# Performance work log

Measured on AMD Instinct MI355X. Metric: run time of the kernel, lower is better.

Reference implementation:

```python
import jax, jax.numpy as jnp
import numpy as np

NP_, NS_ = 100000, 10000      # num pdrugs / seffect nodes
FPD, FSE = 512, 768           # raw feature dims
H = 64                        # hidden_channels
E = 1_600_000                 # message-passing edges
L = 1_000_000                 # labeled edges (pos+neg)


def setup_inputs() -> dict:
    key = jax.random.key(0)
    ks = jax.random.split(key, 40)
    f32 = jnp.float32

    def nrm(k, shape, scale=0.05):
        return jax.random.normal(k, shape, f32) * scale

    inp = {}
    inp['x_pdrugs'] = jax.random.normal(ks[0], (NP_, FPD), f32)
    inp['x_seffect'] = jax.random.normal(ks[1], (NS_, FSE), f32)
    inp['node_id_pd'] = jnp.arange(NP_)
    inp['node_id_se'] = jnp.arange(NS_)
    inp['edge_index'] = jnp.stack([
        jax.random.randint(ks[2], (E,), 0, NP_),
        jax.random.randint(ks[3], (E,), 0, NS_)])
    # positive labeled edges + negative-sampled edges (label 0)
    inp['edge_label_index'] = jnp.stack([
        jax.random.randint(ks[4], (L,), 0, NP_),
        jax.random.randint(ks[5], (L,), 0, NS_)])
    inp['edge_label'] = jnp.concatenate(
        [jnp.ones(L // 2, f32), jnp.zeros(L - L // 2, f32)])

    # input projections + node embeddings
    inp['W_pd'] = nrm(ks[6], (FPD, H)); inp['b_pd'] = jnp.zeros((H,), f32)
    inp['W_se'] = nrm(ks[7], (FSE, H)); inp['b_se'] = jnp.zeros((H,), f32)
    inp['emb_pd'] = nrm(ks[8], (NP_, H), 1.0)
    inp['emb_se'] = nrm(ks[9], (NS_, H), 1.0)

    # hetero SAGEConv params: 2 layers x 2 edge types (p2s, s2p)
    i = 10
    for lyr in (1, 2):
        for et in ('p2s', 's2p'):
            inp[f'c{lyr}_{et}_Wl'] = nrm(ks[i], (H, H)); i += 1
            inp[f'c{lyr}_{et}_bl'] = jnp.zeros((H,), f32)
            inp[f'c{lyr}_{et}_Wr'] = nrm(ks[i], (H, H)); i += 1
    return inp


def _sage(x_src, x_dst, src_idx, dst_idx, n_dst, Wl, bl, Wr):
    # SAGEConv: lin_l(mean_j x_src[j]) + lin_r(x_dst)
    msg = x_src[src_idx]                                   # [E, H] gather
    agg = jax.ops.segment_sum(msg, dst_idx, num_segments=n_dst)
    deg = jax.ops.segment_sum(jnp.ones((src_idx.shape[0],), x_src.dtype),
                              dst_idx, num_segments=n_dst)
    mean = agg / jnp.clip(deg, 1.0)[:, None]
    return mean @ Wl + bl + x_dst @ Wr


def reference(x_pdrugs, x_seffect, edge_label,
              W_pd, b_pd, W_se, b_se, emb_pd, emb_se,
              c1_p2s_Wl, c1_p2s_bl, c1_p2s_Wr,
              c1_s2p_Wl, c1_s2p_bl, c1_s2p_Wr,
              c2_p2s_Wl, c2_p2s_bl, c2_p2s_Wr,
              c2_s2p_Wl, c2_s2p_bl, c2_s2p_Wr,
              node_id_pd, node_id_se, edge_index, edge_label_index):
    src, dst = edge_index[0], edge_index[1]  # pdrugs -> seffect

    # embed + linear fusion
    h_pd = x_pdrugs @ W_pd + b_pd + emb_pd[node_id_pd]
    h_se = x_seffect @ W_se + b_se + emb_se[node_id_se]

    # hetero GNN layer 1 (relu)
    se1 = jax.nn.relu(_sage(h_pd, h_se, src, dst, NS_, c1_p2s_Wl, c1_p2s_bl, c1_p2s_Wr))
    pd1 = jax.nn.relu(_sage(h_se, h_pd, dst, src, NP_, c1_s2p_Wl, c1_s2p_bl, c1_s2p_Wr))

    # hetero GNN layer 2 (no activation)
    se2 = _sage(pd1, se1, src, dst, NS_, c2_p2s_Wl, c2_p2s_bl, c2_p2s_Wr)
    pd2 = _sage(se1, pd1, dst, src, NP_, c2_s2p_Wl, c2_s2p_bl, c2_s2p_Wr)

    # edge-wise gather-dot classifier
    pred = jnp.sum(pd2[edge_label_index[0]] * se2[edge_label_index[1]], axis=-1)
    return (pred, edge_label)
```

## Files before the change

### kernel.cpp

```cpp
#include <hip/hip_runtime.h>

namespace {

constexpr int NP = 100000;
constexpr int NS = 10000;
constexpr int EC = 1600000;
constexpr int LC = 1000000;

constexpr int SH_S = 6;
constexpr int SH_P = 9;
constexpr int NBS = (NS + 63) >> SH_S;
constexpr int NBP = (NP + 511) >> SH_P;
constexpr int CHUNK = 8192;
constexpr int NBLK = (EC + CHUNK - 1) / CHUNK;
constexpr int LBLK = (LC + CHUNK - 1) / CHUNK;

typedef short i16x8 __attribute__((ext_vector_type(8)));
typedef float f32x4 __attribute__((ext_vector_type(4)));

__device__ inline ushort f2bf(float f) {
  unsigned u = __float_as_uint(f);
  u += 0x7FFFu + ((u >> 16) & 1u);
  return (ushort)(u >> 16);
}
__device__ inline float bflo(uint v) { return __uint_as_float(v << 16); }
__device__ inline float bfhi(uint v) { return __uint_as_float(v & 0xffff0000u); }

__device__ inline i16x8 pack8(float4 a, float4 b) {
  i16x8 r;
  r[0] = (short)f2bf(a.x);
  r[1] = (short)f2bf(a.y);
  r[2] = (short)f2bf(a.z);
  r[3] = (short)f2bf(a.w);
  r[4] = (short)f2bf(b.x);
  r[5] = (short)f2bf(b.y);
  r[6] = (short)f2bf(b.z);
  r[7] = (short)f2bf(b.w);
  return r;
}


__global__ void __launch_bounds__(256) k_bcount(const int* __restrict__ src,
                                                const int* __restrict__ dst,
                                                const int* __restrict__ li0,
                                                int* __restrict__ bcntS,
                                                int* __restrict__ bcntP,
                                                int* __restrict__ bcntL, int E, int L) {
  __shared__ int hS[256];
  __shared__ int hP[256];
  const int t = threadIdx.x;
  if ((int)blockIdx.x >= NBLK) {
    hS[t] = 0;
    __syncthreads();
    const int base = ((int)blockIdx.x - NBLK) * CHUNK;
    const int end = min(base + CHUNK, L);
    for (int e = base + t; e < end; e += 256) atomicAdd(&hS[li0[e] >> SH_P], 1);
    __syncthreads();
    if (t < NBP && hS[t]) atomicAdd(&bcntL[t], hS[t]);
    return;
  }
  hS[t] = 0;
  hP[t] = 0;
  __syncthreads();
  const int base = blockIdx.x * CHUNK;
  const int end = min(base + CHUNK, E);
  for (int e = base + t; e < end; e += 256) {
    atomicAdd(&hS[dst[e] >> SH_S], 1);
    atomicAdd(&hP[src[e] >> SH_P], 1);
  }
  __syncthreads();
  if (t < NBS && hS[t]) atomicAdd(&bcntS[t], hS[t]);
  if (t < NBP && hP[t]) atomicAdd(&bcntP[t], hP[t]);
}

__global__ void __launch_bounds__(256) k_bscan(const int* __restrict__ bcntS,
                                               const int* __restrict__ bcntP,
                                               const int* __restrict__ bcntL,
                                               int* __restrict__ gbaseS,
                                               int* __restrict__ gbaseP,
                                               int* __restrict__ gcurS,
                                               int* __restrict__ gcurP,
                                               int* __restrict__ gcurL) {
  __shared__ int s[256];
  const int t = threadIdx.x;
  int v = (t < NBS) ? bcntS[t] : 0;
  s[t] = v;
  __syncthreads();
  for (int off = 1; off < 256; off <<= 1) {
    int u = (t >= off) ? s[t - off] : 0;
    __syncthreads();
    s[t] += u;
    __syncthreads();
  }
  if (t < NBS) {
    int ex = s[t] - v;
    gbaseS[t] = ex;
    gcurS[t] = ex;
  }
  __syncthreads();
  v = (t < NBP) ? bcntP[t] : 0;
  s[t] = v;
  __syncthreads();
  for (int off = 1; off < 256; off <<= 1) {
    int u = (t >= off) ? s[t - off] : 0;
    __syncthreads();
    s[t] += u;
    __syncthreads();
  }
  if (t < NBP) {
    int ex = s[t] - v;
    gbaseP[t] = ex;
    gcurP[t] = ex;
  }
  __syncthreads();
  v = (t < NBP) ? bcntL[t] : 0;
  s[t] = v;
  __syncthreads();
  for (int off = 1; off < 256; off <<= 1) {
    int u = (t >= off) ? s[t - off] : 0;
    __syncthreads();
    s[t] += u;
    __syncthreads();
  }
  if (t < NBP) gcurL[t] = s[t] - v;
}

__global__ void __launch_bounds__(256) k_bscatter(const int* __restrict__ src,
                                                  const int* __restrict__ dst,
                                                  const int* __restrict__ li0,
                                                  int* __restrict__ gcurS,
                                                  int* __restrict__ gcurP,
                                                  int* __restrict__ gcurL,
                                                  int* __restrict__ tmpS,
                                                  int* __restrict__ tmpP,
                                                  int2* __restrict__ tmpL, int E, int L) {
  __shared__ int hS[256];
  __shared__ int hP[256];
  const int t = threadIdx.x;
  if ((int)blockIdx.x >= NBLK) {
    hS[t] = 0;
    __syncthreads();
    const int base = ((int)blockIdx.x - NBLK) * CHUNK;
    const int end = min(base + CHUNK, L);
    for (int e = base + t; e < end; e += 256) atomicAdd(&hS[li0[e] >> SH_P], 1);
    __syncthreads();
    int myBase = 0;
    if (t < NBP) {
      int c = hS[t];
      myBase = c ? atomicAdd(&gcurL[t], c) : 0;
    }
    __syncthreads();
    if (t < NBP) hS[t] = myBase;
    __syncthreads();
    for (int e = base + t; e < end; e += 256) {
      const int a = li0[e];
      int p = atomicAdd(&hS[a >> SH_P], 1);
      tmpL[p] = make_int2(a, e);
    }
    return;
  }
  hS[t] = 0;
  hP[t] = 0;
  __syncthreads();
  const int base = blockIdx.x * CHUNK;
  const int end = min(base + CHUNK, E);
  for (int e = base + t; e < end; e += 256) {
    atomicAdd(&hS[dst[e] >> SH_S], 1);
    atomicAdd(&hP[src[e] >> SH_P], 1);
  }
  __syncthreads();
  int myBaseS = 0, myBaseP = 0;
  if (t < NBS) {
    int c = hS[t];
    myBaseS = c ? atomicAdd(&gcurS[t], c) : 0;
  }
  if (t < NBP) {
    int c = hP[t];
    myBaseP = c ? atomicAdd(&gcurP[t], c) : 0;
  }
  __syncthreads();
  if (t < NBS) hS[t] = myBaseS;
  if (t < NBP) hP[t] = myBaseP;
  __syncthreads();
  for (int e = base + t; e < end; e += 256) {
    const int d = dst[e];
    const int s = src[e];
    int p = atomicAdd(&hS[d >> SH_S], 1);
    tmpS[p] = ((d & 63) << 17) | s;
    int q = atomicAdd(&hP[s >> SH_P], 1);
    tmpP[q] = ((s & 511) << 14) | d;
  }
}

template <int NN, int LBITS>
__global__ void __launch_bounds__(256) k_bfinal(const int* __restrict__ tmp,
                                                const int* __restrict__ gbase,
                                                const int* __restrict__ bcnt,
                                                int shift, int Nnodes,
                                                int* __restrict__ rowptr,
                                                int* __restrict__ deg,
                                                int* __restrict__ col) {
  __shared__ int ldeg[NN];
  __shared__ int lscan[512];
  const int b = blockIdx.x;
  const int t = threadIdx.x;
  const int n0 = b << shift;
  const int base = gbase[b];
  const int cnt = bcnt[b];
  for (int i = t; i < NN; i += 256) ldeg[i] = 0;
  __syncthreads();
  for (int j = t; j < cnt; j += 256) atomicAdd(&ldeg[tmp[base + j] >> LBITS], 1);
  __syncthreads();
  for (int i = t; i < 512; i += 256) lscan[i] = (i < NN) ? ldeg[i] : 0;
  __syncthreads();
  for (int off = 1; off < 512; off <<= 1) {
    const int i0 = t, i1 = t + 256;
    const int v0 = (i0 >= off) ? lscan[i0 - off] : 0;
    const int v1 = (i1 >= off) ? lscan[i1 - off] : 0;
    __syncthreads();
    lscan[i0] += v0;
    lscan[i1] += v1;
    __syncthreads();
  }
  for (int i = t; i < NN; i += 256) {
    const int n = n0 + i;
    if (n < Nnodes) {
      const int dg = ldeg[i];
      rowptr[n] = base + lscan[i] - dg;
      deg[n] = dg;
    }
  }
  __syncthreads();
  for (int i = t; i < NN; i += 256) lscan[i] -= ldeg[i];
  __syncthreads();
  for (int j = t; j < cnt; j += 256) {
    const int v = tmp[base + j];
    const int p = atomicAdd(&lscan[v >> LBITS], 1);
    col[base + p] = v & ((1 << LBITS) - 1);
  }
}


struct WtJob {
  const float* src;
  ushort* dst;
  int K;
  int stride;
  int off;
};
struct WtJobs {
  WtJob j[10];
};

__global__ void __launch_bounds__(256) k_wt_all(WtJobs jobs) {
  int e = blockIdx.x * 256 + threadIdx.x;
#pragma unroll
  for (int i = 0; i < 10; i++) {
    const int K = jobs.j[i].K;
    const int sz = K * 64;
    if (e < sz) {
      const int n = e / K;
      const int k = e - n * K;
      jobs.j[i].dst[(size_t)n * jobs.j[i].stride + jobs.j[i].off + k] =
          f2bf(jobs.j[i].src[(size_t)k * 64 + n]);
      return;
    }
    e -= sz;
  }
}


struct GJob {
  const void* A0;
  const void* A1;
  int KA0, sA0, sA1, K;
  const ushort* Wt;
  const float* bias;
  const float* emb;
  const int* nid;
  void* out;
  int M;
  int nblk;
};

template <bool RELU, bool EMB, bool ABF16, bool OBF16>
__global__ void __launch_bounds__(256) k_fgemm(GJob ja, GJob jb) {
  const bool sec = (int)blockIdx.x >= ja.nblk;
  const GJob j = sec ? jb : ja;
  const int bid = sec ? ((int)blockIdx.x - ja.nblk) : (int)blockIdx.x;
  const int t = threadIdx.x;
  const int lane = t & 63;
  const int w = t >> 6;
  const int m16 = lane & 15;
  const int q = lane >> 4;
  const int M = j.M;
  const int K = j.K;
  const int KA0 = j.KA0;
  const int row0 = bid * 64 + w * 16;
  const int gr = min(row0 + m16, M - 1);

  f32x4 acc[4];
#pragma unroll
  for (int nt = 0; nt < 4; nt++) acc[nt] = {0.f, 0.f, 0.f, 0.f};

  const int ksteps = K >> 6;
#pragma unroll 2
  for (int ks = 0; ks < ksteps; ks++) {
    const int k0 = ks << 6;
    i16x8 a0, a1;
    if constexpr (ABF16) {
      const int ka = k0 + q * 8;
      const ushort* p0 = (ka < KA0)
                             ? ((const ushort*)j.A0 + (size_t)gr * j.sA0 + ka)
                             : ((const ushort*)j.A1 + (size_t)gr * j.sA1 + (ka - KA0));
      const int kb = ka + 32;
      const ushort* p1 = (kb < KA0)
                             ? ((const ushort*)j.A0 + (size_t)gr * j.sA0 + kb)
                             : ((const ushort*)j.A1 + (size_t)gr * j.sA1 + (kb - KA0));
      a0 = *reinterpret_cast<const i16x8*>(p0);
      a1 = *reinterpret_cast<const i16x8*>(p1);
    } else {
      const float* pa = (const float*)j.A0 + (size_t)gr * j.sA0 + k0 + q * 8;
      const float4 f0 = *reinterpret_cast<const float4*>(pa);
      const float4 f1 = *reinterpret_cast<const float4*>(pa + 4);
      const float4 g0 = *reinterpret_cast<const float4*>(pa + 32);
      const float4 g1 = *reinterpret_cast<const float4*>(pa + 36);
      a0 = pack8(f0, f1);
      a1 = pack8(g0, g1);
    }
#pragma unroll
    for (int nt = 0; nt < 4; nt++) {
      const ushort* wb = j.Wt + (size_t)(nt * 16 + m16) * K + k0 + q * 8;
      const i16x8 b0 = *reinterpret_cast<const i16x8*>(wb);
      const i16x8 b1 = *reinterpret_cast<const i16x8*>(wb + 32);
      acc[nt] = __builtin_amdgcn_mfma_f32_16x16x32_bf16(a0, b0, acc[nt], 0, 0, 0);
      acc[nt] = __builtin_amdgcn_mfma_f32_16x16x32_bf16(a1, b1, acc[nt], 0, 0, 0);
    }
  }

  int grow[4];
  int nrow[4];
#pragma unroll
  for (int r = 0; r < 4; r++) {
    grow[r] = bid * 64 + w * 16 + q * 4 + r;
    nrow[r] = (EMB && grow[r] < M) ? j.nid[grow[r]] : 0;
  }
#pragma unroll
  for (int nt = 0; nt < 4; nt++) {
    const int colv = nt * 16 + m16;
    const float bv = j.bias[colv];
#pragma unroll
    for (int r = 0; r < 4; r++) {
      if (grow[r] < M) {
        float v = acc[nt][r] + bv;
        if (EMB) v += j.emb[(size_t)nrow[r] * 64 + colv];
        if (RELU) v = fmaxf(v, 0.f);
        if (OBF16)
          ((ushort*)j.out)[(size_t)grow[r] * 64 + colv] = f2bf(v);
        else
          ((float*)j.out)[(size_t)grow[r] * 64 + colv] = v;
      }
    }
  }
}


__global__ void __launch_bounds__(256) k_agg2(
    const ushort* __restrict__ hS,
    const ushort* __restrict__ hP,
    const int* __restrict__ rpS, const int* __restrict__ degS, const int* __restrict__ colS,
    const int* __restrict__ rpP, const int* __restrict__ degP, const int* __restrict__ colP,
    ushort* __restrict__ outS,
    ushort* __restrict__ outP
) {
  int g = blockIdx.x * 4 + (threadIdx.x >> 6);
  const uint* hu;
  const int* rp;
  const int* deg;
  const int* col;
  uint* out;
  int node;
  if (g < NS) {
    hu = (const uint*)hS; rp = rpS; deg = degS; col = colS; out = (uint*)outS;
    node = g;
  } else {
    node = g - NS;
    if (node >= NP) return;
    hu = (const uint*)hP; rp = rpP; deg = degP; col = colP; out = (uint*)outP;
  }
  const int lane = threadIdx.x & 63;
  const int c = lane & 31;
  const int half = lane >> 5;
  const int beg = rp[node];
  const int cnt = deg[node];
  float a0 = 0.f, a1 = 0.f;
  int jj = 0;
  for (; jj + 16 <= cnt; jj += 16) {
    int n[8];
#pragma unroll
    for (int u = 0; u < 8; u++) n[u] = col[beg + jj + 2 * u + half];
#pragma unroll
    for (int u = 0; u < 8; u++) {
      const uint v = hu[(size_t)n[u] * 32 + c];
      a0 += bflo(v);
      a1 += bfhi(v);
    }
  }
  for (; jj + 2 <= cnt; jj += 2) {
    const uint v = hu[(size_t)col[beg + jj + half] * 32 + c];
    a0 += bflo(v);
    a1 += bfhi(v);
  }
  if (jj < cnt && half == 0) {
    const uint v = hu[(size_t)col[beg + jj] * 32 + c];
    a0 += bflo(v);
    a1 += bfhi(v);
  }
  a0 += __shfl_xor(a0, 32);
  a1 += __shfl_xor(a1, 32);
  if (half == 0) {
    const float d = (cnt > 0) ? (float)cnt : 1.f;
    const uint o = (uint)f2bf(a0 / d) | ((uint)f2bf(a1 / d) << 16);
    out[(size_t)node * 32 + c] = o;
  }
}


__global__ void __launch_bounds__(256) k_classify(const float* __restrict__ pd2,
                                                  const float* __restrict__ se2,
                                                  const int2* __restrict__ tmpL,
                                                  const int* __restrict__ i1,
                                                  const float* __restrict__ elabel,
                                                  float* __restrict__ outF, int L,
                                                  int nClsBlk) {
  if ((int)blockIdx.x >= nClsBlk) {
    const int i = ((int)blockIdx.x - nClsBlk) * 256 + threadIdx.x;
    if (i < L / 4)
      reinterpret_cast<float4*>(outF + L)[i] =
          reinterpret_cast<const float4*>(elabel)[i];
    return;
  }
  const int e = blockIdx.x * 16 + (threadIdx.x >> 4);
  if (e >= L) return;
  const int l16 = threadIdx.x & 15;
  const int2 pr = tmpL[e];
  const int a = pr.x;
  const int idx = pr.y;
  const int b = i1[idx];
  const float4 va = *reinterpret_cast<const float4*>(&pd2[(size_t)a * 64 + l16 * 4]);
  const float4 vb = *reinterpret_cast<const float4*>(&se2[(size_t)b * 64 + l16 * 4]);
  float v = va.x * vb.x + va.y * vb.y + va.z * vb.z + va.w * vb.w;
  v += __shfl_xor(v, 1, 16);
  v += __shfl_xor(v, 2, 16);
  v += __shfl_xor(v, 4, 16);
  v += __shfl_xor(v, 8, 16);
  if (l16 == 0) outF[idx] = v;
}

}

extern "C" void kernel_launch(void* const* d_in, const int* in_sizes, int n_in,
                              void* d_out, int out_size, void* d_ws, size_t ws_size,
                              hipStream_t stream) {
  (void)in_sizes; (void)n_in; (void)out_size; (void)ws_size;
  const float* x_pd = (const float*)d_in[0];
  const float* x_se = (const float*)d_in[1];
  const int* nid_pd = (const int*)d_in[2];
  const int* nid_se = (const int*)d_in[3];
  const int* eidx = (const int*)d_in[4];
  const int* elidx = (const int*)d_in[5];
  const float* elabel = (const float*)d_in[6];
  const float* W_pd = (const float*)d_in[7];
  const float* b_pd = (const float*)d_in[8];
  const float* W_se = (const float*)d_in[9];
  const float* b_se = (const float*)d_in[10];
  const float* emb_pd = (const float*)d_in[11];
  const float* emb_se = (const float*)d_in[12];
  const float* c1_p2s_Wl = (const float*)d_in[13];
  const float* c1_p2s_bl = (const float*)d_in[14];
  const float* c1_p2s_Wr = (const float*)d_in[15];
  const float* c1_s2p_Wl = (const float*)d_in[16];
  const float* c1_s2p_bl = (const float*)d_in[17];
  const float* c1_s2p_Wr = (const float*)d_in[18];
  const float* c2_p2s_Wl = (const float*)d_in[19];
  const float* c2_p2s_bl = (const float*)d_in[20];
  const float* c2_p2s_Wr = (const float*)d_in[21];
  const float* c2_s2p_Wl = (const float*)d_in[22];
  const float* c2_s2p_bl = (const float*)d_in[23];
  const float* c2_s2p_Wr = (const float*)d_in[24];

  const int* src = eidx;
  const int* dst = eidx + EC;
  const int* li0 = elidx;
  const int* li1 = elidx + LC;

  char* ws = (char*)d_ws;
  size_t o = 0;
  auto alloc = [&](size_t bytes) -> char* {
    char* p = ws + o;
    o = (o + bytes + 255) & ~(size_t)255;
    return p;
  };
  ushort* h_pd = (ushort*)alloc((size_t)NP * 64 * 2);
  ushort* h_se = (ushort*)alloc((size_t)NS * 64 * 2);
  ushort* pd1 = (ushort*)alloc((size_t)NP * 64 * 2);
  ushort* se1 = (ushort*)alloc((size_t)NS * 64 * 2);
  ushort* agg_pd = (ushort*)alloc((size_t)NP * 64 * 2);
  ushort* agg_se = (ushort*)alloc((size_t)NS * 64 * 2);
  float* pd2 = (float*)alloc((size_t)NP * 64 * 4);
  float* se2 = (float*)alloc((size_t)NS * 64 * 4);
  int* col_se = (int*)alloc((size_t)EC * 4);
  int* col_pd = (int*)alloc((size_t)EC * 4);
  int2* tmpL = (int2*)alloc((size_t)LC * 8);
  int* deg_se = (int*)alloc((size_t)NS * 4);
  int* deg_pd = (int*)alloc((size_t)NP * 4);
  int* rp_se = (int*)alloc((size_t)NS * 4);
  int* rp_pd = (int*)alloc((size_t)NP * 4);
  int* bcntS = (int*)alloc(1024);
  int* bcntP = (int*)alloc(1024);
  int* bcntL = (int*)alloc(1024);
  int* gbaseS = (int*)alloc(1024);
  int* gbaseP = (int*)alloc(1024);
  int* gcurS = (int*)alloc(1024);
  int* gcurP = (int*)alloc(1024);
  int* gcurL = (int*)alloc(1024);
  ushort* wt_pd = (ushort*)alloc((size_t)64 * 512 * 2);
  ushort* wt_se = (ushort*)alloc((size_t)64 * 768 * 2);
  ushort* wt_c1p2s = (ushort*)alloc((size_t)64 * 128 * 2);
  ushort* wt_c1s2p = (ushort*)alloc((size_t)64 * 128 * 2);
  ushort* wt_c2p2s = (ushort*)alloc((size_t)64 * 128 * 2);
  ushort* wt_c2s2p = (ushort*)alloc((size_t)64 * 128 * 2);

  int* tmpS = (int*)pd2;
  int* tmpP = tmpS + EC;

  hipMemsetAsync(bcntS, 0, 3072, stream);

  k_bcount<<<NBLK + LBLK, 256, 0, stream>>>(src, dst, li0, bcntS, bcntP, bcntL, EC, LC);
  k_bscan<<<1, 256, 0, stream>>>(bcntS, bcntP, bcntL, gbaseS, gbaseP, gcurS, gcurP,
                                 gcurL);
  k_bscatter<<<NBLK + LBLK, 256, 0, stream>>>(src, dst, li0, gcurS, gcurP, gcurL, tmpS,
                                              tmpP, tmpL, EC, LC);
  k_bfinal<64, 17><<<NBS, 256, 0, stream>>>(tmpS, gbaseS, bcntS, SH_S, NS, rp_se,
                                            deg_se, col_se);
  k_bfinal<512, 14><<<NBP, 256, 0, stream>>>(tmpP, gbaseP, bcntP, SH_P, NP, rp_pd,
                                             deg_pd, col_pd);

  {
    WtJobs jobs;
    jobs.j[0] = {W_pd, wt_pd, 512, 512, 0};
    jobs.j[1] = {W_se, wt_se, 768, 768, 0};
    jobs.j[2] = {c1_p2s_Wl, wt_c1p2s, 64, 128, 0};
    jobs.j[3] = {c1_p2s_Wr, wt_c1p2s, 64, 128, 64};
    jobs.j[4] = {c1_s2p_Wl, wt_c1s2p, 64, 128, 0};
    jobs.j[5] = {c1_s2p_Wr, wt_c1s2p, 64, 128, 64};
    jobs.j[6] = {c2_p2s_Wl, wt_c2p2s, 64, 128, 0};
    jobs.j[7] = {c2_p2s_Wr, wt_c2p2s, 64, 128, 64};
    jobs.j[8] = {c2_s2p_Wl, wt_c2s2p, 64, 128, 0};
    jobs.j[9] = {c2_s2p_Wr, wt_c2s2p, 64, 128, 64};
    const int tot = 64 * (512 + 768 + 8 * 64);
    k_wt_all<<<(tot + 255) / 256, 256, 0, stream>>>(jobs);
  }

  const int gP = (NP + 63) / 64;
  const int gS = (NS + 63) / 64;
  const int gAgg = (NS + NP) / 4;

  {
    GJob jp = {x_pd, nullptr, 512, 512, 0, 512, wt_pd, b_pd, emb_pd, nid_pd, h_pd, NP, gP};
    GJob js = {x_se, nullptr, 768, 768, 0, 768, wt_se, b_se, emb_se, nid_se, h_se, NS, gS};
    k_fgemm<false, true, false, true><<<gP + gS, 256, 0, stream>>>(jp, js);
  }

  k_agg2<<<gAgg, 256, 0, stream>>>(h_pd, h_se, rp_se, deg_se, col_se, rp_pd, deg_pd,
                                   col_pd, agg_se, agg_pd);
  {
    GJob jp = {agg_pd, h_pd, 64, 64, 64, 128, wt_c1s2p, c1_s2p_bl, nullptr, nullptr, pd1, NP, gP};
    GJob js = {agg_se, h_se, 64, 64, 64, 128, wt_c1p2s, c1_p2s_bl, nullptr, nullptr, se1, NS, gS};
    k_fgemm<true, false, true, true><<<gP + gS, 256, 0, stream>>>(jp, js);
  }

  k_agg2<<<gAgg, 256, 0, stream>>>(pd1, se1, rp_se, deg_se, col_se, rp_pd, deg_pd,
                                   col_pd, agg_se, agg_pd);
  {
    GJob jp = {agg_pd, pd1, 64, 64, 64, 128, wt_c2s2p, c2_s2p_bl, nullptr, nullptr, pd2, NP, gP};
    GJob js = {agg_se, se1, 64, 64, 64, 128, wt_c2p2s, c2_p2s_bl, nullptr, nullptr, se2, NS, gS};
    k_fgemm<false, false, true, false><<<gP + gS, 256, 0, stream>>>(jp, js);
  }

  float* outF = (float*)d_out;
  const int nClsBlk = (LC + 15) / 16;
  const int nCpyBlk = (LC / 4 + 255) / 256;
  k_classify<<<nClsBlk + nCpyBlk, 256, 0, stream>>>(pd2, se2, tmpL, li1, elabel, outF,
                                                    LC, nClsBlk);
}
```

Measured before the change: 765.6 us.

## Stage A tiles through LDS with coalesced row loads in fused GEMM

The GEMM kernel now loads each 64-row block of A into shared memory using fully coalesced loads across the block, converting fp32 to bf16 during staging. Previously each lane read scattered 16-byte fragments straight into MFMA registers. The change aims to improve global-load coalescing for the large input projection, which reads the 100000x512 fp32 matrix. It adds LDS use and block-wide barriers between K chunks, with no double buffering, so load and compute no longer overlap within a block.

```diff
diff --git a/kernel.cpp b/kernel.cpp
--- a/kernel.cpp
+++ b/kernel.cpp
@@ -25,19 +25,6 @@
 }
 __device__ inline float bflo(uint v) { return __uint_as_float(v << 16); }
 __device__ inline float bfhi(uint v) { return __uint_as_float(v & 0xffff0000u); }
-
-__device__ inline i16x8 pack8(float4 a, float4 b) {
-  i16x8 r;
-  r[0] = (short)f2bf(a.x);
-  r[1] = (short)f2bf(a.y);
-  r[2] = (short)f2bf(a.z);
-  r[3] = (short)f2bf(a.w);
-  r[4] = (short)f2bf(b.x);
-  r[5] = (short)f2bf(b.y);
-  r[6] = (short)f2bf(b.z);
-  r[7] = (short)f2bf(b.w);
-  return r;
-}
 
 
 __global__ void __launch_bounds__(256) k_bcount(const int* __restrict__ src,
@@ -284,7 +271,10 @@
 };
 
 template <bool RELU, bool EMB, bool ABF16, bool OBF16>
-__global__ void __launch_bounds__(256) k_fgemm(GJob ja, GJob jb) {
+__global__ void __launch_bounds__(256) k_sgemm(GJob ja, GJob jb) {
+  constexpr int KC = ABF16 ? 128 : 256;
+  constexpr int LDW = ABF16 ? 136 : 264;
+  __shared__ ushort As[64 * LDW];
   const bool sec = (int)blockIdx.x >= ja.nblk;
   const GJob j = sec ? jb : ja;
   const int bid = sec ? ((int)blockIdx.x - ja.nblk) : (int)blockIdx.x;
@@ -295,46 +285,60 @@
   const int q = lane >> 4;
   const int M = j.M;
   const int K = j.K;
-  const int KA0 = j.KA0;
-  const int row0 = bid * 64 + w * 16;
-  const int gr = min(row0 + m16, M - 1);
+  const int row0 = bid * 64;
 
   f32x4 acc[4];
 #pragma unroll
   for (int nt = 0; nt < 4; nt++) acc[nt] = {0.f, 0.f, 0.f, 0.f};
 
-  const int ksteps = K >> 6;
-#pragma unroll 2
-  for (int ks = 0; ks < ksteps; ks++) {
-    const int k0 = ks << 6;
-    i16x8 a0, a1;
+  const int nst = K / KC;
+  for (int s = 0; s < nst; s++) {
+    const int k0 = s * KC;
+    if (s) __syncthreads();
     if constexpr (ABF16) {
-      const int ka = k0 + q * 8;
-      const ushort* p0 = (ka < KA0)
-                             ? ((const ushort*)j.A0 + (size_t)gr * j.sA0 + ka)
-                             : ((const ushort*)j.A1 + (size_t)gr * j.sA1 + (ka - KA0));
-      const int kb = ka + 32;
-      const ushort* p1 = (kb < KA0)
-                             ? ((const ushort*)j.A0 + (size_t)gr * j.sA0 + kb)
-                             : ((const ushort*)j.A1 + (size_t)gr * j.sA1 + (kb - KA0));
-      a0 = *reinterpret_cast<const i16x8*>(p0);
-      a1 = *reinterpret_cast<const i16x8*>(p1);
+#pragma unroll
+      for (int i = 0; i < 4; i++) {
+        const int u = i * 256 + t;
+        const int row = u >> 4;
+        const int c = u & 15;
+        const int gr = min(row0 + row, M - 1);
+        const ushort* sp = (c < 8)
+                               ? ((const ushort*)j.A0 + (size_t)gr * j.sA0 + c * 8)
+                               : ((const ushort*)j.A1 + (size_t)gr * j.sA1 + (c - 8) * 8);
+        *reinterpret_cast<uint4*>(&As[row * LDW + c * 8]) =
+            *reinterpret_cast<const uint4*>(sp);
+      }
     } else {
-      const float* pa = (const float*)j.A0 + (size_t)gr * j.sA0 + k0 + q * 8;
-      const float4 f0 = *reinterpret_cast<const float4*>(pa);
-      const float4 f1 = *reinterpret_cast<const float4*>(pa + 4);
-      const float4 g0 = *reinterpret_cast<const float4*>(pa + 32);
-      const float4 g1 = *reinterpret_cast<const float4*>(pa + 36);
-      a0 = pack8(f0, f1);
-      a1 = pack8(g0, g1);
-    }
-#pragma unroll
-    for (int nt = 0; nt < 4; nt++) {
-      const ushort* wb = j.Wt + (size_t)(nt * 16 + m16) * K + k0 + q * 8;
-      const i16x8 b0 = *reinterpret_cast<const i16x8*>(wb);
-      const i16x8 b1 = *reinterpret_cast<const i16x8*>(wb + 32);
-      acc[nt] = __builtin_amdgcn_mfma_f32_16x16x32_bf16(a0, b0, acc[nt], 0, 0, 0);
-      acc[nt] = __builtin_amdgcn_mfma_f32_16x16x32_bf16(a1, b1, acc[nt], 0, 0, 0);
+#pragma unroll 8
+      for (int i = 0; i < 16; i++) {
+        const int u = i * 256 + t;
+        const int row = u >> 6;
+        const int c4 = u & 63;
+        const int gr = min(row0 + row, M - 1);
+        const float4 v = *reinterpret_cast<const float4*>(
+            (const float*)j.A0 + (size_t)gr * j.sA0 + k0 + c4 * 4);
+        ushort4 o;
+        o.x = f2bf(v.x);
+        o.y = f2bf(v.y);
+        o.z = f2bf(v.z);
+        o.w = f2bf(v.w);
+        *reinterpret_cast<ushort4*>(&As[row * LDW + c4 * 4]) = o;
+      }
+    }
+    __syncthreads();
+#pragma unroll
+    for (int ks = 0; ks < KC / 64; ks++) {
+      const ushort* ap = &As[(w * 16 + m16) * LDW + ks * 64 + q * 8];
+      const i16x8 a0 = *reinterpret_cast<const i16x8*>(ap);
+      const i16x8 a1 = *reinterpret_cast<const i16x8*>(ap + 32);
+#pragma unroll
+      for (int nt = 0; nt < 4; nt++) {
+        const ushort* wb = j.Wt + (size_t)(nt * 16 + m16) * K + k0 + ks * 64 + q * 8;
+        const i16x8 b0 = *reinterpret_cast<const i16x8*>(wb);
+        const i16x8 b1 = *reinterpret_cast<const i16x8*>(wb + 32);
+        acc[nt] = __builtin_amdgcn_mfma_f32_16x16x32_bf16(a0, b0, acc[nt], 0, 0, 0);
+        acc[nt] = __builtin_amdgcn_mfma_f32_16x16x32_bf16(a1, b1, acc[nt], 0, 0, 0);
+      }
     }
   }
 
@@ -342,7 +346,7 @@
   int nrow[4];
 #pragma unroll
   for (int r = 0; r < 4; r++) {
-    grow[r] = bid * 64 + w * 16 + q * 4 + r;
+    grow[r] = row0 + w * 16 + q * 4 + r;
     nrow[r] = (EMB && grow[r] < M) ? j.nid[grow[r]] : 0;
   }
 #pragma unroll
@@ -569,7 +573,7 @@
   {
     GJob jp = {x_pd, nullptr, 512, 512, 0, 512, wt_pd, b_pd, emb_pd, nid_pd, h_pd, NP, gP};
     GJob js = {x_se, nullptr, 768, 768, 0, 768, wt_se, b_se, emb_se, nid_se, h_se, NS, gS};
-    k_fgemm<false, true, false, true><<<gP + gS, 256, 0, stream>>>(jp, js);
+    k_sgemm<false, true, false, true><<<gP + gS, 256, 0, stream>>>(jp, js);
   }
 
   k_agg2<<<gAgg, 256, 0, stream>>>(h_pd, h_se, rp_se, deg_se, col_se, rp_pd, deg_pd,
@@ -577,7 +581,7 @@
   {
     GJob jp = {agg_pd, h_pd, 64, 64, 64, 128, wt_c1s2p, c1_s2p_bl, nullptr, nullptr, pd1, NP, gP};
     GJob js = {agg_se, h_se, 64, 64, 64, 128, wt_c1p2s, c1_p2s_bl, nullptr, nullptr, se1, NS, gS};
-    k_fgemm<true, false, true, true><<<gP + gS, 256, 0, stream>>>(jp, js);
+    k_sgemm<true, false, true, true><<<gP + gS, 256, 0, stream>>>(jp, js);
   }
 
   k_agg2<<<gAgg, 256, 0, stream>>>(pd1, se1, rp_se, deg_se, col_se, rp_pd, deg_pd,
@@ -585,7 +589,7 @@
   {
     GJob jp = {agg_pd, pd1, 64, 64, 64, 128, wt_c2s2p, c2_s2p_bl, nullptr, nullptr, pd2, NP, gP};
     GJob js = {agg_se, se1, 64, 64, 64, 128, wt_c2p2s, c2_p2s_bl, nullptr, nullptr, se2, NS, gS};
-    k_fgemm<false, false, true, false><<<gP + gS, 256, 0, stream>>>(jp, js);
+    k_sgemm<false, false, true, false><<<gP + gS, 256, 0, stream>>>(jp, js);
   }
 
   float* outF = (float*)d_out;
```

New measurement: 816.1 us. +6.6%, slower.
